# Optimization experiments

Measured on AMD Instinct MI355X. Metric: run time of the kernel, lower is better.

## Reference

```python
import jax, jax.numpy as jnp
import numpy as np

N = 50000          # nodes
E = 1_600_000      # edges (avg degree 32, radius graph capped at 64 nbrs)
F_X = 32           # node feature dim
F_E = 8            # edge attr dim
RADIUS = 8.0       # radius used to normalize pair distance
EPS = 1e-5         # LayerNorm eps (torch default)


def _glorot(key, shape):
    fan_in = shape[0]
    return (jax.random.normal(key, shape, dtype=jnp.float32) / np.sqrt(fan_in)).astype(jnp.float32)


def setup_inputs() -> dict:
    key = jax.random.key(0)
    ks = jax.random.split(key, 16)
    x = jax.random.normal(ks[0], (N, F_X), dtype=jnp.float32)
    pos = jax.random.normal(ks[1], (N, 3), dtype=jnp.float32) * 10.0
    normal = jax.random.normal(ks[2], (N, 3), dtype=jnp.float32)
    normal = normal / jnp.linalg.norm(normal, axis=1, keepdims=True)
    edge_attr = jax.random.normal(ks[3], (E, F_E), dtype=jnp.float32)
    edge_index = jax.random.randint(ks[4], (2, E), 0, N, dtype=jnp.int64)
    d_in = F_X + 7 + F_E  # 47
    return {
        "x": x, "pos": pos, "normal": normal, "edge_attr": edge_attr,
        "edge_index": edge_index,
        # local MLP: [47 -> 64 -> 128], each block Linear->ReLU->LayerNorm
        "W1": _glorot(ks[5], (d_in, 64)), "b1": jnp.zeros((64,), jnp.float32),
        "g1": jnp.ones((64,), jnp.float32), "be1": jnp.zeros((64,), jnp.float32),
        "W2": _glorot(ks[6], (64, 128)), "b2": jnp.zeros((128,), jnp.float32),
        "g2": jnp.ones((128,), jnp.float32), "be2": jnp.zeros((128,), jnp.float32),
        # global MLP: [128 -> 256]
        "Wg": _glorot(ks[7], (128, 256)), "bg": jnp.zeros((256,), jnp.float32),
        "gg": jnp.ones((256,), jnp.float32), "beg": jnp.zeros((256,), jnp.float32),
    }


def _layernorm(h, g, b):
    mu = jnp.mean(h, axis=-1, keepdims=True)
    var = jnp.mean(jnp.square(h - mu), axis=-1, keepdims=True)
    return (h - mu) * jax.lax.rsqrt(var + EPS) * g + b


def _mlp_block(h, W, b, g, be):
    # Linear -> ReLU -> LayerNorm (Dropout inactive in eval mode)
    return _layernorm(jax.nn.relu(h @ W + b), g, be)


def _angle(v1, v2):
    cross = jnp.cross(v1, v2)
    return jnp.arctan2(jnp.linalg.norm(cross, axis=1), jnp.sum(v1 * v2, axis=1))


def reference(x, pos, normal, edge_attr, edge_index,
              W1, b1, g1, be1, W2, b2, g2, be2, Wg, bg, gg, beg):
    src = edge_index[0]  # j (source)
    dst = edge_index[1]  # i (target)
    pos_i, pos_j = pos[dst], pos[src]
    n_i, n_j = normal[dst], normal[src]
    pseudo = pos_j - pos_i                       # [E,3]
    a1 = _angle(n_i, pseudo)
    a2 = _angle(n_j, pseudo)
    a3 = _angle(n_i, n_j)
    ppf = jnp.stack([
        jnp.linalg.norm(pseudo, axis=1) / RADIUS,
        jnp.sin(a1), jnp.cos(a1),
        jnp.sin(a2), jnp.cos(a2),
        jnp.sin(a3), jnp.cos(a3),
    ], axis=1)                                   # [E,7]
    msg = jnp.concatenate([x[src], ppf, edge_attr], axis=1)  # [E,47]
    msg = _mlp_block(msg, W1, b1, g1, be1)       # [E,64]
    msg = _mlp_block(msg, W2, b2, g2, be2)       # [E,128]
    agg = jax.ops.segment_max(msg, dst, num_segments=N)      # [N,128]
    agg = jnp.where(jnp.isfinite(agg), agg, 0.0)  # nodes with no in-edges -> 0
    out = _mlp_block(agg, Wg, bg, gg, beg)       # [N,256]
    return out
```

## Files before the change

kernel.cpp:

```cpp
#include <hip/hip_runtime.h>
#include <hip/hip_bf16.h>
#include <math.h>


#define LN_EPS 1e-5f
#define EPB 128
#define SM 72
#define SP 130
#define AS 132

typedef __attribute__((ext_vector_type(8))) short bf16x8;
typedef __attribute__((ext_vector_type(4))) float floatx4;
typedef __attribute__((ext_vector_type(4))) short s4v;

__device__ __forceinline__ unsigned ord(float f) {
    int i = __float_as_int(f);
    return (i >= 0) ? ((unsigned)i | 0x80000000u) : ~((unsigned)i);
}
__device__ __forceinline__ float unord(unsigned u) {
    int i = (u & 0x80000000u) ? (int)(u & 0x7fffffffu) : ~(int)u;
    return __int_as_float(i);
}
__device__ __forceinline__ unsigned short f2b(float f) {
    unsigned u = __float_as_uint(f);
    return (unsigned short)((u + 0x7FFFu + ((u >> 16) & 1u)) >> 16);
}
__device__ __forceinline__ float b2f(unsigned short h) {
    return __uint_as_float((unsigned)h << 16);
}
__device__ __forceinline__ unsigned f2b2(float lo, float hi) {
    union { __hip_bfloat162 h2; unsigned u; } c;
    c.h2 = __float22bfloat162_rn(make_float2(lo, hi));
    return c.u;
}
__device__ __forceinline__ float b2f_lo(unsigned w) { return __uint_as_float(w << 16); }
__device__ __forceinline__ float b2f_hi(unsigned w) { return __uint_as_float(w & 0xFFFF0000u); }

__global__ void hist_kernel(const int* __restrict__ ei, unsigned* __restrict__ deg, int E) {
    int b4 = (blockIdx.x * 256 + threadIdx.x) * 4;
    if (b4 + 3 < E) {
        int4 d4 = *(const int4*)(ei + E + b4);
        atomicAdd(&deg[d4.x], 1u);
        atomicAdd(&deg[d4.y], 1u);
        atomicAdd(&deg[d4.z], 1u);
        atomicAdd(&deg[d4.w], 1u);
    } else {
        for (int i = 0; i < 4; ++i)
            if (b4 + i < E) atomicAdd(&deg[ei[E + b4 + i]], 1u);
    }
}

__global__ void scan1(const unsigned* __restrict__ deg, unsigned* __restrict__ part, int N) {
    __shared__ unsigned s[256];
    int i = blockIdx.x * 256 + threadIdx.x;
    s[threadIdx.x] = (i < N) ? deg[i] : 0u;
    __syncthreads();
    for (int st = 128; st > 0; st >>= 1) {
        if (threadIdx.x < st) s[threadIdx.x] += s[threadIdx.x + st];
        __syncthreads();
    }
    if (threadIdx.x == 0) part[blockIdx.x] = s[0];
}

__global__ void scan2(unsigned* __restrict__ part, int nb) {
    __shared__ unsigned s[256];
    int t = threadIdx.x;
    unsigned v = (t < nb) ? part[t] : 0u;
    s[t] = v;
    __syncthreads();
    for (int st = 1; st < 256; st <<= 1) {
        unsigned add = (t >= st) ? s[t - st] : 0u;
        __syncthreads();
        s[t] += add;
        __syncthreads();
    }
    if (t < nb) part[t] = s[t] - v;
}

__global__ void scan3(const unsigned* __restrict__ deg, const unsigned* __restrict__ part,
                      unsigned* __restrict__ off, int N) {
    __shared__ unsigned s[256];
    int i = blockIdx.x * 256 + threadIdx.x, t = threadIdx.x;
    unsigned v = (i < N) ? deg[i] : 0u;
    s[t] = v;
    __syncthreads();
    for (int st = 1; st < 256; st <<= 1) {
        unsigned add = (t >= st) ? s[t - st] : 0u;
        __syncthreads();
        s[t] += add;
        __syncthreads();
    }
    if (i < N) off[i] = part[blockIdx.x] + s[t] - v;
}

__global__ void scatter_kernel(const int* __restrict__ ei, unsigned* __restrict__ cursor,
                               uint2* __restrict__ pd, int E) {
    int b4 = (blockIdx.x * 256 + threadIdx.x) * 4;
    if (b4 + 3 < E) {
        int4 d4 = *(const int4*)(ei + E + b4);
        pd[atomicAdd(&cursor[d4.x], 1u)] = make_uint2((unsigned)(b4 + 0), (unsigned)d4.x);
        pd[atomicAdd(&cursor[d4.y], 1u)] = make_uint2((unsigned)(b4 + 1), (unsigned)d4.y);
        pd[atomicAdd(&cursor[d4.z], 1u)] = make_uint2((unsigned)(b4 + 2), (unsigned)d4.z);
        pd[atomicAdd(&cursor[d4.w], 1u)] = make_uint2((unsigned)(b4 + 3), (unsigned)d4.w);
    } else {
        for (int i = 0; i < 4; ++i)
            if (b4 + i < E) {
                int d = ei[E + b4 + i];
                pd[atomicAdd(&cursor[d], 1u)] = make_uint2((unsigned)(b4 + i), (unsigned)d);
            }
    }
}

__global__ void wprep_kernel(const float* __restrict__ W1, const float* __restrict__ W2,
                             const float* __restrict__ Wg,
                             unsigned short* __restrict__ W1p, unsigned short* __restrict__ W2p,
                             unsigned short* __restrict__ Wgp)
{
    int gt = blockIdx.x * 256 + threadIdx.x;
    int gs = gridDim.x * 256;
    for (int fl = gt; fl < 8 * 64; fl += gs) {
        int fi = fl >> 6, l = fl & 63;
        int s = fi >> 2, nt = fi & 3;
        int n = nt * 16 + (l & 15);
        int kb = s * 32 + ((l >> 4) << 3);
        #pragma unroll
        for (int j = 0; j < 8; ++j) {
            int k = kb + j;
            W1p[fl * 8 + j] = f2b((k < 47) ? W1[k * 64 + n] : 0.f);
        }
    }
    for (int fl = gt; fl < 16 * 64; fl += gs) {
        int fi = fl >> 6, l = fl & 63;
        int s = fi >> 3, nt = fi & 7;
        int n = nt * 16 + (l & 15);
        int kb = s * 32 + ((l >> 4) << 3);
        #pragma unroll
        for (int j = 0; j < 8; ++j)
            W2p[fl * 8 + j] = f2b(W2[(kb + j) * 128 + n]);
    }
    for (int fl = gt; fl < 64 * 64; fl += gs) {
        int fi = fl >> 6, l = fl & 63;
        int s = fi >> 4, nt = fi & 15;
        int n = nt * 16 + (l & 15);
        int kb = s * 32 + ((l >> 4) << 3);
        #pragma unroll
        for (int j = 0; j < 8; ++j)
            Wgp[fl * 8 + j] = f2b(Wg[(size_t)(kb + j) * 256 + n]);
    }
}

__global__ __launch_bounds__(256, 3)
void edge_kernel(const float* __restrict__ x,
                 const float* __restrict__ pos,
                 const float* __restrict__ nrm,
                 const float* __restrict__ ea,
                 const int* __restrict__ ei,
                 const uint2* __restrict__ pd,
                 const unsigned short* __restrict__ W1p, const float* __restrict__ b1,
                 const float* __restrict__ g1, const float* __restrict__ be1,
                 const unsigned short* __restrict__ W2p, const float* __restrict__ b2,
                 const float* __restrict__ g2, const float* __restrict__ be2,
                 unsigned* __restrict__ agg, int E)
{
    __shared__ unsigned short hbuf[EPB * SM];
    __shared__ unsigned short st[128 * SP];
    __shared__ int dloc[EPB];
    __shared__ short rstart[EPB], rend[EPB];
    __shared__ unsigned long long wmask[2];
    __shared__ int dprev_s, dnext_s;

    const int tid  = threadIdx.x;
    const int lane = tid & 63;
    const int half = tid >> 7;
    const int el   = tid & 127;
    const int base = blockIdx.x * EPB;
    const int p    = base + el;
    const bool valid = p < E;
    const int nvalid = (E - base < EPB) ? (E - base) : EPB;

    int dst = 0, src = 0, e = 0;
    if (valid) {
        uint2 pv = pd[p];
        e   = (int)pv.x;
        dst = (int)pv.y;
        src = ei[e];
    }
    if (half == 0) dloc[el] = valid ? dst : -1;
    if (tid == 0)
        dprev_s = (blockIdx.x == 0) ? -1 : (int)pd[(size_t)base - 1].y;
    if (tid == 1)
        dnext_s = (base + EPB < E) ? (int)pd[base + EPB].y : -1;

    if (valid) {
        unsigned short* row = &hbuf[el * SM];
        if (half == 0) {
            const float4* xp = (const float4*)(x + (size_t)src * 32);
            #pragma unroll
            for (int q = 0; q < 4; ++q) {
                float4 v = xp[q];
                *(uint2*)&row[4 * q] = make_uint2(f2b2(v.x, v.y), f2b2(v.z, v.w));
            }
            float pix = pos[3*dst+0], piy = pos[3*dst+1], piz = pos[3*dst+2];
            float pjx = pos[3*src+0], pjy = pos[3*src+1], pjz = pos[3*src+2];
            float dx = pjx - pix, dy = pjy - piy, dz = pjz - piz;
            float nix = nrm[3*dst+0], niy = nrm[3*dst+1], niz = nrm[3*dst+2];
            float njx = nrm[3*src+0], njy = nrm[3*src+1], njz = nrm[3*src+2];
            row[32] = f2b(sqrtf(dx*dx + dy*dy + dz*dz) * 0.125f);
            float cx, cy, cz, c2, d, den, inv, sn, cs;
            cx = niy*dz - niz*dy; cy = niz*dx - nix*dz; cz = nix*dy - niy*dx;
            c2 = cx*cx + cy*cy + cz*cz;  d = nix*dx + niy*dy + niz*dz;
            den = c2 + d*d;
            if (den > 0.f) { inv = rsqrtf(den); sn = sqrtf(c2)*inv; cs = d*inv; }
            else           { sn = 0.f; cs = 1.f; }
            row[33] = f2b(sn); row[34] = f2b(cs);
            cx = njy*dz - njz*dy; cy = njz*dx - njx*dz; cz = njx*dy - njy*dx;
            c2 = cx*cx + cy*cy + cz*cz;  d = njx*dx + njy*dy + njz*dz;
            den = c2 + d*d;
            if (den > 0.f) { inv = rsqrtf(den); sn = sqrtf(c2)*inv; cs = d*inv; }
            else           { sn = 0.f; cs = 1.f; }
            row[35] = f2b(sn); row[36] = f2b(cs);
            cx = niy*njz - niz*njy; cy = niz*njx - nix*njz; cz = nix*njy - niy*njx;
            c2 = cx*cx + cy*cy + cz*cz;  d = nix*njx + niy*njy + niz*njz;
            den = c2 + d*d;
            if (den > 0.f) { inv = rsqrtf(den); sn = sqrtf(c2)*inv; cs = d*inv; }
            else           { sn = 0.f; cs = 1.f; }
            row[37] = f2b(sn); row[38] = f2b(cs);
        } else {
            const float4* xp = (const float4*)(x + (size_t)src * 32) + 4;
            #pragma unroll
            for (int q = 0; q < 4; ++q) {
                float4 v = xp[q];
                *(uint2*)&row[16 + 4 * q] = make_uint2(f2b2(v.x, v.y), f2b2(v.z, v.w));
            }
            const float4* ep = (const float4*)(ea + (size_t)e * 8);
            float4 a0 = ep[0], a1 = ep[1];
            row[39] = f2b(a0.x);
            *(uint2*)&row[40] = make_uint2(f2b2(a0.y, a0.z), f2b2(a0.w, a1.x));
            *(uint2*)&row[44] = make_uint2(f2b2(a1.y, a1.z), f2b2(a1.w, 0.f));
            uint2 z = make_uint2(0u, 0u);
            *(uint2*)&row[48] = z; *(uint2*)&row[52] = z;
            *(uint2*)&row[56] = z; *(uint2*)&row[60] = z;
        }
    }
    __syncthreads();

    bool is_start = false, is_end = false;
    if (tid < 128) {
        int dt = dloc[tid];
        bool isv = tid < nvalid;
        is_start = isv && (tid == 0 || dloc[tid - 1] != dt);
        is_end   = isv && (tid == nvalid - 1 || dloc[tid + 1] != dt);
    }
    {
        unsigned long long mb = __ballot(is_start);
        if ((tid >> 6) < 2 && lane == 0) wmask[tid >> 6] = mb;
    }
    __syncthreads();
    int nr;
    {
        unsigned long long m0 = wmask[0], m1 = wmask[1];
        nr = __popcll(m0) + __popcll(m1);
        if (tid < 128) {
            int widr = tid >> 6;
            int rid = (widr ? __popcll(m0) : 0)
                    + __popcll((widr ? m1 : m0) & ((1ull << lane) - 1ull));
            if (is_start) rstart[rid] = (short)tid;
            if (is_end)   rend[is_start ? rid : rid - 1] = (short)tid;
        }
    }

    const int wid  = __builtin_amdgcn_readfirstlane(tid >> 6);
    const int quad = lane >> 4, col = lane & 15;
    const int mb0  = wid * 32;

    {
        bf16x8 w1f[8];
        const bf16x8* W1v = (const bf16x8*)W1p;
        #pragma unroll
        for (int i = 0; i < 8; ++i) w1f[i] = W1v[i * 64 + lane];
        float b1v[4], g1v[4], e1v[4];
        #pragma unroll
        for (int nt = 0; nt < 4; ++nt) {
            b1v[nt] = b1[nt*16 + col]; g1v[nt] = g1[nt*16 + col]; e1v[nt] = be1[nt*16 + col];
        }
        #pragma unroll
        for (int t = 0; t < 2; ++t) {
            const int mb = mb0 + t * 16;
            floatx4 acc[4] = {{0,0,0,0},{0,0,0,0},{0,0,0,0},{0,0,0,0}};
            #pragma unroll
            for (int s = 0; s < 2; ++s) {
                const unsigned short* ap = &hbuf[(mb + col) * SM + s*32 + quad*8];
                union { s4v h[2]; bf16x8 v; } u;
                u.h[0] = *(const s4v*)ap; u.h[1] = *(const s4v*)(ap + 4);
                #pragma unroll
                for (int nt = 0; nt < 4; ++nt)
                    acc[nt] = __builtin_amdgcn_mfma_f32_16x16x32_bf16(u.v, w1f[s*4+nt], acc[nt], 0, 0, 0);
            }
            float ps[4] = {0,0,0,0}, p2[4] = {0,0,0,0};
            #pragma unroll
            for (int nt = 0; nt < 4; ++nt)
                #pragma unroll
                for (int r = 0; r < 4; ++r) {
                    float v = fmaxf(acc[nt][r] + b1v[nt], 0.f);
                    acc[nt][r] = v; ps[r] += v; p2[r] += v * v;
                }
            #pragma unroll
            for (int r = 0; r < 4; ++r) {
                #pragma unroll
                for (int m = 1; m < 16; m <<= 1) {
                    ps[r] += __shfl_xor(ps[r], m);
                    p2[r] += __shfl_xor(p2[r], m);
                }
            }
            float mu[4], rs[4];
            #pragma unroll
            for (int r = 0; r < 4; ++r) {
                mu[r] = ps[r] * (1.f/64.f);
                float var = fmaxf(p2[r] * (1.f/64.f) - mu[r]*mu[r], 0.f);
                rs[r] = rsqrtf(var + LN_EPS);
            }
            #pragma unroll
            for (int nt = 0; nt < 4; ++nt) {
                #pragma unroll
                for (int r = 0; r < 4; r += 2) {
                    float h0 = (acc[nt][r]   - mu[r])   * rs[r]   * g1v[nt] + e1v[nt];
                    float h1 = (acc[nt][r+1] - mu[r+1]) * rs[r+1] * g1v[nt] + e1v[nt];
                    unsigned pk = f2b2(h0, h1);
                    hbuf[(mb + quad*4 + r)   * SM + nt*16 + col] = (unsigned short)pk;
                    hbuf[(mb + quad*4 + r+1) * SM + nt*16 + col] = (unsigned short)(pk >> 16);
                }
            }
        }
    }
    {
        bf16x8 w2f[16];
        const bf16x8* W2v = (const bf16x8*)W2p;
        #pragma unroll
        for (int i = 0; i < 16; ++i) w2f[i] = W2v[i * 64 + lane];
        float b2v[8], g2v[8], e2v[8];
        #pragma unroll
        for (int nt = 0; nt < 8; ++nt) {
            b2v[nt] = b2[nt*16 + col]; g2v[nt] = g2[nt*16 + col]; e2v[nt] = be2[nt*16 + col];
        }
        #pragma unroll
        for (int t = 0; t < 2; ++t) {
            const int mb = mb0 + t * 16;
            floatx4 acc[8] = {{0,0,0,0},{0,0,0,0},{0,0,0,0},{0,0,0,0},
                              {0,0,0,0},{0,0,0,0},{0,0,0,0},{0,0,0,0}};
            #pragma unroll
            for (int s = 0; s < 2; ++s) {
                const unsigned short* ap = &hbuf[(mb + col) * SM + s*32 + quad*8];
                union { s4v h[2]; bf16x8 v; } u;
                u.h[0] = *(const s4v*)ap; u.h[1] = *(const s4v*)(ap + 4);
                #pragma unroll
                for (int nt = 0; nt < 8; ++nt)
                    acc[nt] = __builtin_amdgcn_mfma_f32_16x16x32_bf16(u.v, w2f[s*8+nt], acc[nt], 0, 0, 0);
            }
            float ps[4] = {0,0,0,0}, p2[4] = {0,0,0,0};
            #pragma unroll
            for (int nt = 0; nt < 8; ++nt)
                #pragma unroll
                for (int r = 0; r < 4; ++r) {
                    float v = fmaxf(acc[nt][r] + b2v[nt], 0.f);
                    acc[nt][r] = v; ps[r] += v; p2[r] += v * v;
                }
            #pragma unroll
            for (int r = 0; r < 4; ++r) {
                #pragma unroll
                for (int m = 1; m < 16; m <<= 1) {
                    ps[r] += __shfl_xor(ps[r], m);
                    p2[r] += __shfl_xor(p2[r], m);
                }
            }
            float mu[4], rs[4];
            #pragma unroll
            for (int r = 0; r < 4; ++r) {
                mu[r] = ps[r] * (1.f/128.f);
                float var = fmaxf(p2[r] * (1.f/128.f) - mu[r]*mu[r], 0.f);
                rs[r] = rsqrtf(var + LN_EPS);
            }
            #pragma unroll
            for (int nt = 0; nt < 8; ++nt) {
                float h0 = (acc[nt][0] - mu[0]) * rs[0] * g2v[nt] + e2v[nt];
                float h1 = (acc[nt][1] - mu[1]) * rs[1] * g2v[nt] + e2v[nt];
                float h2 = (acc[nt][2] - mu[2]) * rs[2] * g2v[nt] + e2v[nt];
                float h3 = (acc[nt][3] - mu[3]) * rs[3] * g2v[nt] + e2v[nt];
                unsigned* d32 = (unsigned*)&st[(nt*16 + col) * SP + mb + quad*4];
                d32[0] = f2b2(h0, h1);
                d32[1] = f2b2(h2, h3);
            }
        }
    }
    __syncthreads();

    {
        const int grp = tid >> 7;
        const int f   = tid & 127;
        const unsigned short* fr = &st[f * SP];
        const unsigned* fp = (const unsigned*)fr;
        for (int r = grp; r < nr; r += 2) {
            int s0 = rstart[r], en = rend[r];
            int d  = dloc[s0];
            float v0 = -1e30f, v1 = -1e30f;
            int c = s0;
            if (c & 1) { v0 = fmaxf(v0, b2f(fr[c])); ++c; }
            for (; c + 3 <= en; c += 4) {
                unsigned wa = fp[c >> 1], wb = fp[(c >> 1) + 1];
                v0 = fmaxf(v0, fmaxf(b2f_lo(wa), b2f_hi(wa)));
                v1 = fmaxf(v1, fmaxf(b2f_lo(wb), b2f_hi(wb)));
            }
            if (c + 1 <= en) {
                unsigned wa = fp[c >> 1];
                v0 = fmaxf(v0, fmaxf(b2f_lo(wa), b2f_hi(wa)));
                c += 2;
            }
            if (c <= en) v0 = fmaxf(v0, b2f(fr[c]));
            float val = fmaxf(v0, v1);
            bool contPrev = (s0 == 0) && (dprev_s == d);
            bool contNext = (en == nvalid - 1) && (dnext_s == d);
            unsigned enc = ord(val);
            unsigned* ap = agg + (size_t)d * 128 + f;
            if (contPrev || contNext) atomicMax(ap, enc);
            else                      *ap = enc;
        }
    }
}

__global__ __launch_bounds__(256, 4)
void node_kernel(const unsigned* __restrict__ agg,
                 const unsigned short* __restrict__ Wgp, const float* __restrict__ bg,
                 const float* __restrict__ gg, const float* __restrict__ beg,
                 float* __restrict__ out, int N)
{
    __shared__ unsigned short a_bf[64 * AS];
    const int tid  = threadIdx.x;
    const int base = blockIdx.x * 64;
    const size_t total = (size_t)N * 128;

    #pragma unroll
    for (int i = 0; i < 32; ++i) {
        int idx = tid + i * 256;
        int nl = idx >> 7, k = idx & 127;
        size_t g = (size_t)base * 128 + idx;
        unsigned u = (g < total) ? agg[g] : 0u;
        a_bf[nl * AS + k] = (u == 0u) ? (unsigned short)0 : f2b(unord(u));
    }
    __syncthreads();

    const int lane = tid & 63;
    const int wid  = __builtin_amdgcn_readfirstlane(tid >> 6);
    const int quad = lane >> 4, col = lane & 15;
    const int m0   = wid * 16;

    bf16x8 af[4];
    #pragma unroll
    for (int s = 0; s < 4; ++s) {
        const unsigned short* ap = &a_bf[(m0 + col) * AS + s*32 + quad*8];
        union { s4v h[2]; bf16x8 v; } u;
        u.h[0] = *(const s4v*)ap; u.h[1] = *(const s4v*)(ap + 4);
        af[s] = u.v;
    }

    float accv[16][4];
    float ps[4] = {0,0,0,0}, p2[4] = {0,0,0,0};
    const bf16x8* Wv = (const bf16x8*)Wgp;
    #pragma unroll
    for (int nt = 0; nt < 16; ++nt) {
        floatx4 acc = {0, 0, 0, 0};
        #pragma unroll
        for (int s = 0; s < 4; ++s)
            acc = __builtin_amdgcn_mfma_f32_16x16x32_bf16(af[s], Wv[(s*16 + nt)*64 + lane], acc, 0, 0, 0);
        float b = bg[nt*16 + col];
        #pragma unroll
        for (int r = 0; r < 4; ++r) {
            float v = fmaxf(acc[r] + b, 0.f);
            accv[nt][r] = v; ps[r] += v; p2[r] += v * v;
        }
    }
    #pragma unroll
    for (int r = 0; r < 4; ++r) {
        #pragma unroll
        for (int m = 1; m < 16; m <<= 1) {
            ps[r] += __shfl_xor(ps[r], m);
            p2[r] += __shfl_xor(p2[r], m);
        }
    }
    float mu[4], rs[4];
    #pragma unroll
    for (int r = 0; r < 4; ++r) {
        mu[r] = ps[r] * (1.f/256.f);
        float var = fmaxf(p2[r] * (1.f/256.f) - mu[r]*mu[r], 0.f);
        rs[r] = rsqrtf(var + LN_EPS);
    }
    #pragma unroll
    for (int nt = 0; nt < 16; ++nt) {
        float g = gg[nt*16 + col], be = beg[nt*16 + col];
        #pragma unroll
        for (int r = 0; r < 4; ++r) {
            int node = base + m0 + quad*4 + r;
            if (node < N)
                out[(size_t)node * 256 + nt*16 + col] = (accv[nt][r] - mu[r]) * rs[r] * g + be;
        }
    }
}

extern "C" void kernel_launch(void* const* d_in, const int* in_sizes, int n_in,
                              void* d_out, int out_size, void* d_ws, size_t ws_size,
                              hipStream_t stream) {
    const float* x         = (const float*)d_in[0];
    const float* pos       = (const float*)d_in[1];
    const float* nrm       = (const float*)d_in[2];
    const float* edge_attr = (const float*)d_in[3];
    const int*   ei        = (const int*)d_in[4];
    const float* W1  = (const float*)d_in[5];
    const float* b1  = (const float*)d_in[6];
    const float* g1  = (const float*)d_in[7];
    const float* be1 = (const float*)d_in[8];
    const float* W2  = (const float*)d_in[9];
    const float* b2  = (const float*)d_in[10];
    const float* g2  = (const float*)d_in[11];
    const float* be2 = (const float*)d_in[12];
    const float* Wg  = (const float*)d_in[13];
    const float* bg  = (const float*)d_in[14];
    const float* gg  = (const float*)d_in[15];
    const float* beg = (const float*)d_in[16];

    const int E = in_sizes[3] / 8;
    const int N = in_sizes[0] / 32;

    char* ws = (char*)d_ws;
    unsigned* agg  = (unsigned*)ws;                   ws += (size_t)N * 128 * 4;
    unsigned* deg  = (unsigned*)ws;                   ws += (size_t)N * 4;
    unsigned* off  = (unsigned*)ws;                   ws += (size_t)N * 4;
    unsigned* part = (unsigned*)ws;                   ws += 256 * 4;
    uint2*    pd   = (uint2*)ws;                      ws += (size_t)E * 8;
    unsigned short* W1p = (unsigned short*)ws;        ws += 8 * 64 * 8 * 2;
    unsigned short* W2p = (unsigned short*)ws;        ws += 16 * 64 * 8 * 2;
    unsigned short* Wgp = (unsigned short*)ws;        ws += 64 * 64 * 8 * 2;

    hipMemsetAsync(agg, 0, (size_t)N * 128 * 4, stream);
    hipMemsetAsync(deg, 0, (size_t)N * 4, stream);

    hipLaunchKernelGGL(wprep_kernel, dim3(16), dim3(256), 0, stream, W1, W2, Wg, W1p, W2p, Wgp);

    const int nbN = (N + 255) / 256;
    const int nbE4 = (E + 1023) / 1024;
    hipLaunchKernelGGL(hist_kernel, dim3(nbE4), dim3(256), 0, stream, ei, deg, E);
    hipLaunchKernelGGL(scan1, dim3(nbN), dim3(256), 0, stream, deg, part, N);
    hipLaunchKernelGGL(scan2, dim3(1), dim3(256), 0, stream, part, nbN);
    hipLaunchKernelGGL(scan3, dim3(nbN), dim3(256), 0, stream, deg, part, off, N);
    hipLaunchKernelGGL(scatter_kernel, dim3(nbE4), dim3(256), 0, stream, ei, off, pd, E);

    hipLaunchKernelGGL(edge_kernel, dim3((E + EPB - 1) / EPB), dim3(256), 0, stream,
                       x, pos, nrm, edge_attr, ei, pd,
                       W1p, b1, g1, be1, W2p, b2, g2, be2, agg, E);

    hipLaunchKernelGGL(node_kernel, dim3((N + 63) / 64), dim3(256), 0, stream,
                       agg, Wgp, bg, gg, beg, (float*)d_out, N);
}
```

Measured before the change: 575.9 us.

## Alias segment-max staging onto hbuf in two column chunks; fuse wprep into hist

Drops the separate 128x130 bf16 staging buffer in the edge kernel. Layer-2 outputs are held in registers and staged into the reused hbuf in two 64-feature halves, each followed by a segment-max pass, which raises the occupancy target from 3 to 4 blocks per CU. The weight-prep kernel is also merged into the histogram launch as extra blocks to save one launch. In exchange there are extra barriers, more live registers (pk2), and a pressure risk under the tighter launch bound.

```diff
diff --git a/kernel.cpp b/kernel.cpp
--- a/kernel.cpp
+++ b/kernel.cpp
@@ -6,7 +6,7 @@
 #define LN_EPS 1e-5f
 #define EPB 128
 #define SM 72
-#define SP 130
+#define SC 130
 #define AS 132
 
 typedef __attribute__((ext_vector_type(8))) short bf16x8;
@@ -36,7 +36,47 @@
 __device__ __forceinline__ float b2f_lo(unsigned w) { return __uint_as_float(w << 16); }
 __device__ __forceinline__ float b2f_hi(unsigned w) { return __uint_as_float(w & 0xFFFF0000u); }
 
-__global__ void hist_kernel(const int* __restrict__ ei, unsigned* __restrict__ deg, int E) {
+__global__ void hist_wprep_kernel(const int* __restrict__ ei, unsigned* __restrict__ deg, int E,
+                                  int nbHist,
+                                  const float* __restrict__ W1, const float* __restrict__ W2,
+                                  const float* __restrict__ Wg,
+                                  unsigned short* __restrict__ W1p, unsigned short* __restrict__ W2p,
+                                  unsigned short* __restrict__ Wgp)
+{
+    if ((int)blockIdx.x >= nbHist) {
+        int gt = ((int)blockIdx.x - nbHist) * 256 + threadIdx.x;
+        int gs = 16 * 256;
+        for (int fl = gt; fl < 8 * 64; fl += gs) {
+            int fi = fl >> 6, l = fl & 63;
+            int s = fi >> 2, nt = fi & 3;
+            int n = nt * 16 + (l & 15);
+            int kb = s * 32 + ((l >> 4) << 3);
+            #pragma unroll
+            for (int j = 0; j < 8; ++j) {
+                int k = kb + j;
+                W1p[fl * 8 + j] = f2b((k < 47) ? W1[k * 64 + n] : 0.f);
+            }
+        }
+        for (int fl = gt; fl < 16 * 64; fl += gs) {
+            int fi = fl >> 6, l = fl & 63;
+            int s = fi >> 3, nt = fi & 7;
+            int n = nt * 16 + (l & 15);
+            int kb = s * 32 + ((l >> 4) << 3);
+            #pragma unroll
+            for (int j = 0; j < 8; ++j)
+                W2p[fl * 8 + j] = f2b(W2[(kb + j) * 128 + n]);
+        }
+        for (int fl = gt; fl < 64 * 64; fl += gs) {
+            int fi = fl >> 6, l = fl & 63;
+            int s = fi >> 4, nt = fi & 15;
+            int n = nt * 16 + (l & 15);
+            int kb = s * 32 + ((l >> 4) << 3);
+            #pragma unroll
+            for (int j = 0; j < 8; ++j)
+                Wgp[fl * 8 + j] = f2b(Wg[(size_t)(kb + j) * 256 + n]);
+        }
+        return;
+    }
     int b4 = (blockIdx.x * 256 + threadIdx.x) * 4;
     if (b4 + 3 < E) {
         int4 d4 = *(const int4*)(ei + E + b4);
@@ -111,45 +151,7 @@
     }
 }
 
-__global__ void wprep_kernel(const float* __restrict__ W1, const float* __restrict__ W2,
-                             const float* __restrict__ Wg,
-                             unsigned short* __restrict__ W1p, unsigned short* __restrict__ W2p,
-                             unsigned short* __restrict__ Wgp)
-{
-    int gt = blockIdx.x * 256 + threadIdx.x;
-    int gs = gridDim.x * 256;
-    for (int fl = gt; fl < 8 * 64; fl += gs) {
-        int fi = fl >> 6, l = fl & 63;
-        int s = fi >> 2, nt = fi & 3;
-        int n = nt * 16 + (l & 15);
-        int kb = s * 32 + ((l >> 4) << 3);
-        #pragma unroll
-        for (int j = 0; j < 8; ++j) {
-            int k = kb + j;
-            W1p[fl * 8 + j] = f2b((k < 47) ? W1[k * 64 + n] : 0.f);
-        }
-    }
-    for (int fl = gt; fl < 16 * 64; fl += gs) {
-        int fi = fl >> 6, l = fl & 63;
-        int s = fi >> 3, nt = fi & 7;
-        int n = nt * 16 + (l & 15);
-        int kb = s * 32 + ((l >> 4) << 3);
-        #pragma unroll
-        for (int j = 0; j < 8; ++j)
-            W2p[fl * 8 + j] = f2b(W2[(kb + j) * 128 + n]);
-    }
-    for (int fl = gt; fl < 64 * 64; fl += gs) {
-        int fi = fl >> 6, l = fl & 63;
-        int s = fi >> 4, nt = fi & 15;
-        int n = nt * 16 + (l & 15);
-        int kb = s * 32 + ((l >> 4) << 3);
-        #pragma unroll
-        for (int j = 0; j < 8; ++j)
-            Wgp[fl * 8 + j] = f2b(Wg[(size_t)(kb + j) * 256 + n]);
-    }
-}
-
-__global__ __launch_bounds__(256, 3)
+__global__ __launch_bounds__(256, 4)
 void edge_kernel(const float* __restrict__ x,
                  const float* __restrict__ pos,
                  const float* __restrict__ nrm,
@@ -163,11 +165,11 @@
                  unsigned* __restrict__ agg, int E)
 {
     __shared__ unsigned short hbuf[EPB * SM];
-    __shared__ unsigned short st[128 * SP];
     __shared__ int dloc[EPB];
     __shared__ short rstart[EPB], rend[EPB];
     __shared__ unsigned long long wmask[2];
     __shared__ int dprev_s, dnext_s;
+    unsigned short* stc = hbuf;
 
     const int tid  = threadIdx.x;
     const int lane = tid & 63;
@@ -332,6 +334,7 @@
             }
         }
     }
+    unsigned pk2[2][8][2];
     {
         bf16x8 w2f[16];
         const bf16x8* W2v = (const bf16x8*)W2p;
@@ -385,44 +388,59 @@
                 float h1 = (acc[nt][1] - mu[1]) * rs[1] * g2v[nt] + e2v[nt];
                 float h2 = (acc[nt][2] - mu[2]) * rs[2] * g2v[nt] + e2v[nt];
                 float h3 = (acc[nt][3] - mu[3]) * rs[3] * g2v[nt] + e2v[nt];
-                unsigned* d32 = (unsigned*)&st[(nt*16 + col) * SP + mb + quad*4];
-                d32[0] = f2b2(h0, h1);
-                d32[1] = f2b2(h2, h3);
-            }
-        }
-    }
-    __syncthreads();
-
-    {
-        const int grp = tid >> 7;
-        const int f   = tid & 127;
-        const unsigned short* fr = &st[f * SP];
-        const unsigned* fp = (const unsigned*)fr;
-        for (int r = grp; r < nr; r += 2) {
-            int s0 = rstart[r], en = rend[r];
-            int d  = dloc[s0];
-            float v0 = -1e30f, v1 = -1e30f;
-            int c = s0;
-            if (c & 1) { v0 = fmaxf(v0, b2f(fr[c])); ++c; }
-            for (; c + 3 <= en; c += 4) {
-                unsigned wa = fp[c >> 1], wb = fp[(c >> 1) + 1];
-                v0 = fmaxf(v0, fmaxf(b2f_lo(wa), b2f_hi(wa)));
-                v1 = fmaxf(v1, fmaxf(b2f_lo(wb), b2f_hi(wb)));
-            }
-            if (c + 1 <= en) {
-                unsigned wa = fp[c >> 1];
-                v0 = fmaxf(v0, fmaxf(b2f_lo(wa), b2f_hi(wa)));
-                c += 2;
-            }
-            if (c <= en) v0 = fmaxf(v0, b2f(fr[c]));
-            float val = fmaxf(v0, v1);
-            bool contPrev = (s0 == 0) && (dprev_s == d);
-            bool contNext = (en == nvalid - 1) && (dnext_s == d);
-            unsigned enc = ord(val);
-            unsigned* ap = agg + (size_t)d * 128 + f;
-            if (contPrev || contNext) atomicMax(ap, enc);
-            else                      *ap = enc;
-        }
+                pk2[t][nt][0] = f2b2(h0, h1);
+                pk2[t][nt][1] = f2b2(h2, h3);
+            }
+        }
+    }
+    __syncthreads();
+
+    #pragma unroll
+    for (int ch = 0; ch < 2; ++ch) {
+        #pragma unroll
+        for (int t = 0; t < 2; ++t) {
+            const int mb = mb0 + t * 16;
+            #pragma unroll
+            for (int j = 0; j < 4; ++j) {
+                int f = j * 16 + col;
+                unsigned* d32 = (unsigned*)&stc[f * SC + mb + quad*4];
+                d32[0] = pk2[t][ch*4 + j][0];
+                d32[1] = pk2[t][ch*4 + j][1];
+            }
+        }
+        __syncthreads();
+        {
+            const int grp = tid >> 6;
+            const int f   = tid & 63;
+            const unsigned short* fr = &stc[f * SC];
+            const unsigned* fp = (const unsigned*)fr;
+            for (int r = grp; r < nr; r += 4) {
+                int s0 = rstart[r], en = rend[r];
+                int d  = dloc[s0];
+                float v0 = -1e30f, v1 = -1e30f;
+                int c = s0;
+                if (c & 1) { v0 = fmaxf(v0, b2f(fr[c])); ++c; }
+                for (; c + 3 <= en; c += 4) {
+                    unsigned wa = fp[c >> 1], wb = fp[(c >> 1) + 1];
+                    v0 = fmaxf(v0, fmaxf(b2f_lo(wa), b2f_hi(wa)));
+                    v1 = fmaxf(v1, fmaxf(b2f_lo(wb), b2f_hi(wb)));
+                }
+                if (c + 1 <= en) {
+                    unsigned wa = fp[c >> 1];
+                    v0 = fmaxf(v0, fmaxf(b2f_lo(wa), b2f_hi(wa)));
+                    c += 2;
+                }
+                if (c <= en) v0 = fmaxf(v0, b2f(fr[c]));
+                float val = fmaxf(v0, v1);
+                bool contPrev = (s0 == 0) && (dprev_s == d);
+                bool contNext = (en == nvalid - 1) && (dnext_s == d);
+                unsigned enc = ord(val);
+                unsigned* ap = agg + (size_t)d * 128 + ch * 64 + f;
+                if (contPrev || contNext) atomicMax(ap, enc);
+                else                      *ap = enc;
+            }
+        }
+        __syncthreads();
     }
 }
 
@@ -541,11 +559,10 @@
     hipMemsetAsync(agg, 0, (size_t)N * 128 * 4, stream);
     hipMemsetAsync(deg, 0, (size_t)N * 4, stream);
 
-    hipLaunchKernelGGL(wprep_kernel, dim3(16), dim3(256), 0, stream, W1, W2, Wg, W1p, W2p, Wgp);
-
     const int nbN = (N + 255) / 256;
     const int nbE4 = (E + 1023) / 1024;
-    hipLaunchKernelGGL(hist_kernel, dim3(nbE4), dim3(256), 0, stream, ei, deg, E);
+    hipLaunchKernelGGL(hist_wprep_kernel, dim3(nbE4 + 16), dim3(256), 0, stream,
+                       ei, deg, E, nbE4, W1, W2, Wg, W1p, W2p, Wgp);
     hipLaunchKernelGGL(scan1, dim3(nbN), dim3(256), 0, stream, deg, part, N);
     hipLaunchKernelGGL(scan2, dim3(1), dim3(256), 0, stream, part, nbN);
     hipLaunchKernelGGL(scan3, dim3(nbN), dim3(256), 0, stream, deg, part, off, N);
```

Result: slower. 617.0 us (+7.1%).
